# Kernel optimization log

Measured on AMD Instinct MI355X. Metric: run time of the kernel, lower is better.

The kernel has to match this reference:

```python
import jax, jax.numpy as jnp
import numpy as np

N_FRAMES = 20000
N_BEADS = 50


def _feature_indices(n_beads):
    # cgnet's get_distance_indices ordering: by pair separation, then start index
    dist = np.array([(i, i + inc) for inc in range(1, n_beads)
                     for i in range(n_beads - inc)], dtype=np.int32)
    ang = np.array([(i, i + 1, i + 2) for i in range(n_beads - 2)], dtype=np.int32)
    dih = np.array([(i, i + 1, i + 2, i + 3) for i in range(n_beads - 3)], dtype=np.int32)
    return dist, ang, dih


def setup_inputs() -> dict:
    key = jax.random.key(0)
    data = jax.random.normal(key, (N_FRAMES, N_BEADS, 3), dtype=jnp.float32) * 3.0
    return {"data": data}


def reference(data):
    # data: [n_frames, n_beads, 3]
    n_beads = data.shape[1]
    dist_inds, ang_inds, dih_inds = _feature_indices(n_beads)

    # --- pairwise distances: ||x_j - x_i|| -> [F, n_dist]
    dvec = data[:, dist_inds[:, 1]] - data[:, dist_inds[:, 0]]
    distances = jnp.linalg.norm(dvec, axis=-1)

    # --- planar angles at middle bead j of (i, j, k) -> [F, n_ang]
    b1 = data[:, ang_inds[:, 0]] - data[:, ang_inds[:, 1]]
    b2 = data[:, ang_inds[:, 2]] - data[:, ang_inds[:, 1]]
    cos_theta = jnp.sum(b1 * b2, axis=-1) / (
        jnp.linalg.norm(b1, axis=-1) * jnp.linalg.norm(b2, axis=-1))
    angles = jnp.arccos(jnp.clip(cos_theta, -1.0, 1.0))

    # --- dihedrals of (i, j, k, l): cross-product plane normals -> cos, sin
    a = data[:, dih_inds[:, 1]] - data[:, dih_inds[:, 0]]
    b = data[:, dih_inds[:, 2]] - data[:, dih_inds[:, 1]]
    c = data[:, dih_inds[:, 3]] - data[:, dih_inds[:, 2]]
    p1 = jnp.cross(a, b)          # normal of plane (i,j,k)
    p2 = jnp.cross(b, c)          # normal of plane (j,k,l)
    n1 = jnp.linalg.norm(p1, axis=-1)
    n2 = jnp.linalg.norm(p2, axis=-1)
    dih_cos = jnp.sum(p1 * p2, axis=-1) / (n1 * n2)
    dih_sin = jnp.sum(jnp.cross(p1, p2) * b, axis=-1) / (
        n1 * n2 * jnp.linalg.norm(b, axis=-1))

    # description_order: Distances, Angles, Dihedral_cosines, Dihedral_sines
    return jnp.concatenate([distances, angles, dih_cos, dih_sin], axis=1)
```

## Files before the change

### kernel.cpp

```cpp
#include <hip/hip_runtime.h>
#include <math.h>

#define N_FRAMES 20000
#define N_BEADS  50
#define N_DIST   1225
#define N_ANG    48
#define N_DIH    47
#define OUT_STRIDE (N_DIST + N_ANG + 2 * N_DIH)
#define FPB      8
#define FRAME_F  (N_BEADS * 3)
#define FRAME_P  (N_BEADS * 4)

__device__ __forceinline__ int cum_pairs(int inc) {
    return (inc - 1) * 50 - ((inc - 1) * inc) / 2;
}

__device__ __forceinline__ float fsqrt_fast(float x) { return __builtin_amdgcn_sqrtf(x); }
__device__ __forceinline__ float frsq_fast(float x)  { return __builtin_amdgcn_rsqf(x); }

__global__ __launch_bounds__(256, 6)
void protein_feat_kernel(const float* __restrict__ data, float* __restrict__ out) {
    const int tid = threadIdx.x;
    const int f0  = blockIdx.x * FPB;

    __shared__ __align__(16) float s[FPB * FRAME_P];

    const float4* g4 = (const float4*)(data + (size_t)f0 * FRAME_F);
    float4 v0 = g4[tid];
    const bool h2 = (tid + 256) < (FPB * FRAME_F / 4);
    float4 v1;
    if (h2) v1 = g4[tid + 256];

    int bi_idx[5], bj_idx[5];
#pragma unroll
    for (int k = 0; k < 5; ++k) {
        int p = tid + k * 256;
        if (p < N_DIST) {
            float disc = 9801.0f - 8.0f * (float)p;
            int inc = (int)((101.0f - sqrtf(disc)) * 0.5f);
            inc = min(max(inc, 1), 49);
            while (inc < 49 && cum_pairs(inc + 1) <= p) ++inc;
            while (inc > 1  && cum_pairs(inc)     >  p) --inc;
            int i = p - cum_pairs(inc);
            bi_idx[k] = i;
            bj_idx[k] = i + inc;
        } else {
            bi_idx[k] = 0; bj_idx[k] = 0;
        }
    }
    const bool has_tail = (1024 + tid) < N_DIST;

    {
        int gi = 4 * tid;
#pragma unroll
        for (int c = 0; c < 4; ++c) {
            int B  = (gi + c) / 3;
            int cc = (gi + c) - 3 * B;
            s[B * 4 + cc] = (&v0.x)[c];
        }
        if (h2) {
            int gj = 4 * (tid + 256);
#pragma unroll
            for (int c = 0; c < 4; ++c) {
                int B  = (gj + c) / 3;
                int cc = (gj + c) - 3 * B;
                s[B * 4 + cc] = (&v1.x)[c];
            }
        }
    }
    __syncthreads();

#pragma unroll 1
    for (int f = 0; f < FPB; ++f) {
        const float4* sf4 = (const float4*)s + f * N_BEADS;
        float* fout = out + (size_t)(f0 + f) * OUT_STRIDE;
#pragma unroll
        for (int k = 0; k < 4; ++k) {
            float4 bi = sf4[bi_idx[k]];
            float4 bj = sf4[bj_idx[k]];
            float dx = bj.x - bi.x;
            float dy = bj.y - bi.y;
            float dz = bj.z - bi.z;
            fout[tid + k * 256] = fsqrt_fast(dx * dx + dy * dy + dz * dz);
        }
        if (has_tail) {
            float4 bi = sf4[bi_idx[4]];
            float4 bj = sf4[bj_idx[4]];
            float dx = bj.x - bi.x;
            float dy = bj.y - bi.y;
            float dz = bj.z - bi.z;
            fout[tid + 1024] = fsqrt_fast(dx * dx + dy * dy + dz * dz);
        }
    }

#pragma unroll 1
    for (int idx = tid; idx < FPB * N_ANG; idx += 256) {
        int f = idx / N_ANG;
        int a = idx - f * N_ANG;
        const float4* sf4 = (const float4*)s + f * N_BEADS;
        float4 A = sf4[a], B = sf4[a + 1], C = sf4[a + 2];
        float b1x = A.x - B.x, b1y = A.y - B.y, b1z = A.z - B.z;
        float b2x = C.x - B.x, b2y = C.y - B.y, b2z = C.z - B.z;
        float dot = b1x * b2x + b1y * b2y + b1z * b2z;
        float s1 = b1x * b1x + b1y * b1y + b1z * b1z;
        float s2 = b2x * b2x + b2y * b2y + b2z * b2z;
        float c = dot * frsq_fast(s1 * s2);
        c = fminf(1.0f, fmaxf(-1.0f, c));
        out[(size_t)(f0 + f) * OUT_STRIDE + N_DIST + a] = acosf(c);
    }

#pragma unroll 1
    for (int idx = tid; idx < FPB * N_DIH; idx += 256) {
        int f = idx / N_DIH;
        int d = idx - f * N_DIH;
        const float4* sf4 = (const float4*)s + f * N_BEADS;
        float4 P0 = sf4[d], P1 = sf4[d + 1], P2 = sf4[d + 2], P3 = sf4[d + 3];

        float ax = P1.x - P0.x, ay = P1.y - P0.y, az = P1.z - P0.z;
        float bx = P2.x - P1.x, by = P2.y - P1.y, bz = P2.z - P1.z;
        float cx = P3.x - P2.x, cy = P3.y - P2.y, cz = P3.z - P2.z;

        float p1x = ay * bz - az * by;
        float p1y = az * bx - ax * bz;
        float p1z = ax * by - ay * bx;
        float p2x = by * cz - bz * cy;
        float p2y = bz * cx - bx * cz;
        float p2z = bx * cy - by * cx;

        float s1 = p1x * p1x + p1y * p1y + p1z * p1z;
        float s2 = p2x * p2x + p2y * p2y + p2z * p2z;
        float sb = bx * bx + by * by + bz * bz;

        float dotp = p1x * p2x + p1y * p2y + p1z * p2z;
        float qx = p1y * p2z - p1z * p2y;
        float qy = p1z * p2x - p1x * p2z;
        float qz = p1x * p2y - p1y * p2x;
        float trip = qx * bx + qy * by + qz * bz;

        float inv12 = frsq_fast(s1 * s2);
        float invb  = frsq_fast(sb);
        size_t base = (size_t)(f0 + f) * OUT_STRIDE + N_DIST + N_ANG;
        out[base + d]         = dotp * inv12;
        out[base + N_DIH + d] = trip * inv12 * invb;
    }
}

extern "C" void kernel_launch(void* const* d_in, const int* in_sizes, int n_in,
                              void* d_out, int out_size, void* d_ws, size_t ws_size,
                              hipStream_t stream) {
    const float* data = (const float*)d_in[0];
    float* out = (float*)d_out;
    protein_feat_kernel<<<N_FRAMES / FPB, 256, 0, stream>>>(data, out);
}
```

Before: 123.1 us.

## Stage output rows in LDS and write them back with coalesced float4 stores

Results for each half of the block's frames (4 frames) are now computed into a shared-memory output buffer, then copied to global memory as contiguous float4 stores. The old code wrote scattered scalar stores per feature section. The change aims at fuller, wider write transactions on an output-bound kernel. In exchange it adds about 21KB of LDS, two extra barriers per half and a lower occupancy hint (launch bounds 5 instead of 6).

```diff
diff --git a/kernel.cpp b/kernel.cpp
--- a/kernel.cpp
+++ b/kernel.cpp
@@ -8,6 +8,7 @@
 #define N_DIH    47
 #define OUT_STRIDE (N_DIST + N_ANG + 2 * N_DIH)
 #define FPB      8
+#define HALF     4
 #define FRAME_F  (N_BEADS * 3)
 #define FRAME_P  (N_BEADS * 4)
 
@@ -18,12 +19,13 @@
 __device__ __forceinline__ float fsqrt_fast(float x) { return __builtin_amdgcn_sqrtf(x); }
 __device__ __forceinline__ float frsq_fast(float x)  { return __builtin_amdgcn_rsqf(x); }
 
-__global__ __launch_bounds__(256, 6)
+__global__ __launch_bounds__(256, 5)
 void protein_feat_kernel(const float* __restrict__ data, float* __restrict__ out) {
     const int tid = threadIdx.x;
     const int f0  = blockIdx.x * FPB;
 
     __shared__ __align__(16) float s[FPB * FRAME_P];
+    __shared__ __align__(16) float sout[HALF * OUT_STRIDE];
 
     const float4* g4 = (const float4*)(data + (size_t)f0 * FRAME_F);
     float4 v0 = g4[tid];
@@ -71,77 +73,93 @@
     __syncthreads();
 
 #pragma unroll 1
-    for (int f = 0; f < FPB; ++f) {
-        const float4* sf4 = (const float4*)s + f * N_BEADS;
-        float* fout = out + (size_t)(f0 + f) * OUT_STRIDE;
-#pragma unroll
-        for (int k = 0; k < 4; ++k) {
-            float4 bi = sf4[bi_idx[k]];
-            float4 bj = sf4[bj_idx[k]];
-            float dx = bj.x - bi.x;
-            float dy = bj.y - bi.y;
-            float dz = bj.z - bi.z;
-            fout[tid + k * 256] = fsqrt_fast(dx * dx + dy * dy + dz * dz);
-        }
-        if (has_tail) {
-            float4 bi = sf4[bi_idx[4]];
-            float4 bj = sf4[bj_idx[4]];
-            float dx = bj.x - bi.x;
-            float dy = bj.y - bi.y;
-            float dz = bj.z - bi.z;
-            fout[tid + 1024] = fsqrt_fast(dx * dx + dy * dy + dz * dz);
-        }
-    }
+    for (int half = 0; half < 2; ++half) {
+        const int fbase = half * HALF;
 
 #pragma unroll 1
-    for (int idx = tid; idx < FPB * N_ANG; idx += 256) {
-        int f = idx / N_ANG;
-        int a = idx - f * N_ANG;
-        const float4* sf4 = (const float4*)s + f * N_BEADS;
-        float4 A = sf4[a], B = sf4[a + 1], C = sf4[a + 2];
-        float b1x = A.x - B.x, b1y = A.y - B.y, b1z = A.z - B.z;
-        float b2x = C.x - B.x, b2y = C.y - B.y, b2z = C.z - B.z;
-        float dot = b1x * b2x + b1y * b2y + b1z * b2z;
-        float s1 = b1x * b1x + b1y * b1y + b1z * b1z;
-        float s2 = b2x * b2x + b2y * b2y + b2z * b2z;
-        float c = dot * frsq_fast(s1 * s2);
-        c = fminf(1.0f, fmaxf(-1.0f, c));
-        out[(size_t)(f0 + f) * OUT_STRIDE + N_DIST + a] = acosf(c);
-    }
+        for (int fl = 0; fl < HALF; ++fl) {
+            const float4* sf4 = (const float4*)s + (fbase + fl) * N_BEADS;
+            float* fo = sout + fl * OUT_STRIDE;
+#pragma unroll
+            for (int k = 0; k < 4; ++k) {
+                float4 bi = sf4[bi_idx[k]];
+                float4 bj = sf4[bj_idx[k]];
+                float dx = bj.x - bi.x;
+                float dy = bj.y - bi.y;
+                float dz = bj.z - bi.z;
+                fo[tid + k * 256] = fsqrt_fast(dx * dx + dy * dy + dz * dz);
+            }
+            if (has_tail) {
+                float4 bi = sf4[bi_idx[4]];
+                float4 bj = sf4[bj_idx[4]];
+                float dx = bj.x - bi.x;
+                float dy = bj.y - bi.y;
+                float dz = bj.z - bi.z;
+                fo[tid + 1024] = fsqrt_fast(dx * dx + dy * dy + dz * dz);
+            }
+        }
 
+        if (tid < HALF * N_ANG) {
+            int fl = tid / N_ANG;
+            int a  = tid - fl * N_ANG;
+            const float4* sf4 = (const float4*)s + (fbase + fl) * N_BEADS;
+            float4 A = sf4[a], B = sf4[a + 1], C = sf4[a + 2];
+            float b1x = A.x - B.x, b1y = A.y - B.y, b1z = A.z - B.z;
+            float b2x = C.x - B.x, b2y = C.y - B.y, b2z = C.z - B.z;
+            float dot = b1x * b2x + b1y * b2y + b1z * b2z;
+            float s1 = b1x * b1x + b1y * b1y + b1z * b1z;
+            float s2 = b2x * b2x + b2y * b2y + b2z * b2z;
+            float c = dot * frsq_fast(s1 * s2);
+            c = fminf(1.0f, fmaxf(-1.0f, c));
+            sout[fl * OUT_STRIDE + N_DIST + a] = acosf(c);
+        }
+
+        if (tid < HALF * N_DIH) {
+            int fl = tid / N_DIH;
+            int d  = tid - fl * N_DIH;
+            const float4* sf4 = (const float4*)s + (fbase + fl) * N_BEADS;
+            float4 P0 = sf4[d], P1 = sf4[d + 1], P2 = sf4[d + 2], P3 = sf4[d + 3];
+
+            float ax = P1.x - P0.x, ay = P1.y - P0.y, az = P1.z - P0.z;
+            float bx = P2.x - P1.x, by = P2.y - P1.y, bz = P2.z - P1.z;
+            float cx = P3.x - P2.x, cy = P3.y - P2.y, cz = P3.z - P2.z;
+
+            float p1x = ay * bz - az * by;
+            float p1y = az * bx - ax * bz;
+            float p1z = ax * by - ay * bx;
+            float p2x = by * cz - bz * cy;
+            float p2y = bz * cx - bx * cz;
+            float p2z = bx * cy - by * cx;
+
+            float s1 = p1x * p1x + p1y * p1y + p1z * p1z;
+            float s2 = p2x * p2x + p2y * p2y + p2z * p2z;
+            float sb = bx * bx + by * by + bz * bz;
+
+            float dotp = p1x * p2x + p1y * p2y + p1z * p2z;
+            float qx = p1y * p2z - p1z * p2y;
+            float qy = p1z * p2x - p1x * p2z;
+            float qz = p1x * p2y - p1y * p2x;
+            float trip = qx * bx + qy * by + qz * bz;
+
+            float inv12 = frsq_fast(s1 * s2);
+            float invb  = frsq_fast(sb);
+            float* base = sout + fl * OUT_STRIDE + N_DIST + N_ANG;
+            base[d]         = dotp * inv12;
+            base[N_DIH + d] = trip * inv12 * invb;
+        }
+
+        __syncthreads();
+
+        {
+            const float4* src4 = (const float4*)sout;
+            float4* dst4 = (float4*)(out + (size_t)(f0 + fbase) * OUT_STRIDE);
 #pragma unroll 1
-    for (int idx = tid; idx < FPB * N_DIH; idx += 256) {
-        int f = idx / N_DIH;
-        int d = idx - f * N_DIH;
-        const float4* sf4 = (const float4*)s + f * N_BEADS;
-        float4 P0 = sf4[d], P1 = sf4[d + 1], P2 = sf4[d + 2], P3 = sf4[d + 3];
+            for (int x = tid; x < HALF * OUT_STRIDE / 4; x += 256) {
+                dst4[x] = src4[x];
+            }
+        }
 
-        float ax = P1.x - P0.x, ay = P1.y - P0.y, az = P1.z - P0.z;
-        float bx = P2.x - P1.x, by = P2.y - P1.y, bz = P2.z - P1.z;
-        float cx = P3.x - P2.x, cy = P3.y - P2.y, cz = P3.z - P2.z;
-
-        float p1x = ay * bz - az * by;
-        float p1y = az * bx - ax * bz;
-        float p1z = ax * by - ay * bx;
-        float p2x = by * cz - bz * cy;
-        float p2y = bz * cx - bx * cz;
-        float p2z = bx * cy - by * cx;
-
-        float s1 = p1x * p1x + p1y * p1y + p1z * p1z;
-        float s2 = p2x * p2x + p2y * p2y + p2z * p2z;
-        float sb = bx * bx + by * by + bz * bz;
-
-        float dotp = p1x * p2x + p1y * p2y + p1z * p2z;
-        float qx = p1y * p2z - p1z * p2y;
-        float qy = p1z * p2x - p1x * p2z;
-        float qz = p1x * p2y - p1y * p2x;
-        float trip = qx * bx + qy * by + qz * bz;
-
-        float inv12 = frsq_fast(s1 * s2);
-        float invb  = frsq_fast(sb);
-        size_t base = (size_t)(f0 + f) * OUT_STRIDE + N_DIST + N_ANG;
-        out[base + d]         = dotp * inv12;
-        out[base + N_DIH + d] = trip * inv12 * invb;
+        __syncthreads();
     }
 }
 
```

Measured after the change: 124.1 us. No clear change (+0.8%).
